# Kernel optimization log

Measured on AMD Instinct MI355X. Metric: run time of the kernel, lower is better.

Reference implementation:

```python
import jax, jax.numpy as jnp
import numpy as np

B = 2048            # number of session graphs in the batch
ORDER = 3           # multi-order granularities s1, s2, s3
D = 128             # input_dim = hidden_dim = output_dim (fc_out is None)
NODES_PER = (50, 25, 16)   # nodes per graph for s1, s2, s3
NPG = sum(NODES_PER)       # 91 nodes per graph (summed batch_num_nodes)
N = B * NPG                # total flattened nodes


def setup_inputs() -> dict:
    key = jax.random.key(0)
    k0, k1, k2, k3 = jax.random.split(key, 4)
    feats = jax.random.normal(k0, (N, D), dtype=jnp.float32)
    scale = 1.0 / np.sqrt(D).astype(np.float32)
    Wu = jax.random.normal(k1, (ORDER, D, D), dtype=jnp.float32) * scale
    bu = jnp.zeros((ORDER, D), dtype=jnp.float32)
    Wv = jax.random.normal(k2, (ORDER, D, D), dtype=jnp.float32) * scale
    We = jax.random.normal(k3, (ORDER, D), dtype=jnp.float32) * scale
    # segment id per node: idx = cat([ones(batch_num_nodes[j]) * j])
    idx = jnp.repeat(jnp.arange(B, dtype=jnp.int32), NPG)
    # last node of each order's block inside every graph (feats['s_i'][last_nodess[i]])
    offs = np.cumsum([0] + list(NODES_PER))
    last = np.stack([np.arange(B) * NPG + (offs[o + 1] - 1) for o in range(ORDER)])
    last_idx = jnp.asarray(last, dtype=jnp.int32)  # [ORDER, B]
    return {"feats": feats, "Wu": Wu, "bu": bu, "Wv": Wv, "We": We,
            "idx": idx, "last_idx": last_idx}


def reference(feats, Wu, bu, Wv, We, idx, last_idx):
    # feat_u = fc_u[i](feats)                        -> [O, N, D]
    feat_u = jnp.einsum('nd,odh->onh', feats, Wu) + bu[:, None, :]
    # feat_v = fc_v[i](feat_vs[:, i])[idx]           -> [O, N, D]
    fv = jnp.einsum('obd,odh->obh', feats[last_idx], Wv)   # [O, B, D]
    feat_v = fv[:, idx, :]                                  # gather per segment id
    # e = fc_e[i](sigmoid(feat_u + feat_v))          -> [N, O]
    e = jnp.einsum('onh,oh->no', jax.nn.sigmoid(feat_u + feat_v), We)
    # alpha = segment_softmax(batch_num_nodes, e), numerically stable
    m = jax.lax.stop_gradient(jax.ops.segment_max(e, idx, num_segments=B))
    ex = jnp.exp(e - m[idx])
    denom = jax.ops.segment_sum(ex, idx, num_segments=B)
    alpha = ex / denom[idx]                                 # [N, O]
    # rst = segment_reduce(batch_num_nodes, feats * alpha, 'sum') -> [B, O, D]
    weighted = alpha[:, :, None] * feats[:, None, :]        # [N, O, D]
    rst = jax.ops.segment_sum(weighted, idx, num_segments=B)
    return rst  # [B, ORDER, D]; fc_out is None and activation is None
```

## Files before the change

### kernel.cpp

```cpp
#include <hip/hip_runtime.h>
#include <hip/hip_bf16.h>
#include <stdint.h>

#define NB 2048
#define D 128
#define NPG 91

typedef __attribute__((ext_vector_type(8))) short short8;
typedef __attribute__((ext_vector_type(4))) float f32x4;

__device__ __forceinline__ unsigned bf16pk(float a, float b) {
  __hip_bfloat162 h2 = __float22bfloat162_rn(make_float2(a, b));
  return *reinterpret_cast<unsigned*>(&h2);
}

__device__ __forceinline__ float sigf(float x) {
  float e = __expf(-x);
  return __builtin_amdgcn_rcpf(1.0f + e);
}

__global__ void fv_kernel(const float* __restrict__ feats,
                          const float* __restrict__ Wv,
                          const float* __restrict__ bu,
                          const int* __restrict__ last_idx,
                          float* __restrict__ fv) {
  __shared__ float rows[16][128];
  __shared__ int lidx[16];
  const int o = blockIdx.y;
  const int b0 = blockIdx.x * 16;
  const int t = threadIdx.x;
  if (t < 16) lidx[t] = last_idx[o * NB + b0 + t];
  __syncthreads();
  #pragma unroll
  for (int i = 0; i < 8; ++i) {
    int el = t + i * 256;
    int r = el >> 7, d = el & 127;
    rows[r][d] = feats[(size_t)lidx[r] * D + d];
  }
  __syncthreads();
  const int h = t & 127, half = t >> 7;
  float acc[8];
  #pragma unroll
  for (int j = 0; j < 8; ++j) acc[j] = 0.f;
  const float* wvo = Wv + (size_t)o * D * D + h;
  for (int d0 = 0; d0 < D; d0 += 4) {
    float w0 = wvo[(d0 + 0) * D], w1 = wvo[(d0 + 1) * D];
    float w2 = wvo[(d0 + 2) * D], w3 = wvo[(d0 + 3) * D];
    #pragma unroll
    for (int j = 0; j < 8; ++j) {
      const float4 f = *(const float4*)&rows[half * 8 + j][d0];
      acc[j] += f.x * w0 + f.y * w1 + f.z * w2 + f.w * w3;
    }
  }
  const float bb = bu[o * D + h];
  #pragma unroll
  for (int j = 0; j < 8; ++j)
    fv[((size_t)o * NB + b0 + half * 8 + j) * D + h] = acc[j] + bb;
}

__global__ void wut_pack(const float* __restrict__ Wu, uint4* __restrict__ wupk) {
  const int o = blockIdx.x >> 2, kk = blockIdx.x & 3;
  const int t = threadIdx.x;
  #pragma unroll
  for (int i = 0; i < 2; ++i) {
    int idx = i * 256 + t;
    int row = idx >> 2, g = idx & 3;
    const float* src = Wu + (size_t)o * D * D + (kk * 32 + g * 8) * D + row;
    uint4 pk;
    pk.x = bf16pk(src[0 * D], src[1 * D]);
    pk.y = bf16pk(src[2 * D], src[3 * D]);
    pk.z = bf16pk(src[4 * D], src[5 * D]);
    pk.w = bf16pk(src[6 * D], src[7 * D]);
    wupk[(size_t)blockIdx.x * 512 + idx] = pk;
  }
}

__global__ __launch_bounds__(512, 8) void sihg_main(
    const float* __restrict__ feats,
    const uint4* __restrict__ wupk,
    const float* __restrict__ We,
    const float* __restrict__ fvb,
    float* __restrict__ out) {
  __shared__ __align__(16) char lds[38016];
  constexpr int FE_OFF  = 0;
  constexpr int BFV_OFF = 24576;
  constexpr int WEL_OFF = 26112;
  constexpr int EP_OFF  = 27648;
  constexpr int AL_OFF  = 36864;

  const int t = threadIdx.x;
  const int b = blockIdx.x;
  const int q = t >> 6;
  const int l = t & 63;
  const int g = l >> 4;
  const int lm = l & 15;

  float* bfvp = (float*)(lds + BFV_OFF);
  float* wel = (float*)(lds + WEL_OFF);
  float (*ep)[3][96] = (float (*)[3][96])(lds + EP_OFF);
  float (*alpha)[96] = (float (*)[96])(lds + AL_OFF);

  const float* fbase = feats + (size_t)b * NPG * D;

  #pragma unroll 1
  for (int i = 0; i < 3; ++i) {
    int c = t + i * 512;
    int r = c >> 4, d0 = (c & 15) * 8;
    uint4 pk4;
    if (r < NPG) {
      const float* src = fbase + r * D + d0;
      float4 f0 = *(const float4*)(src);
      float4 f1 = *(const float4*)(src + 4);
      pk4.x = bf16pk(f0.x, f0.y);
      pk4.y = bf16pk(f0.z, f0.w);
      pk4.z = bf16pk(f1.x, f1.y);
      pk4.w = bf16pk(f1.z, f1.w);
    } else {
      pk4.x = 0u; pk4.y = 0u; pk4.z = 0u; pk4.w = 0u;
    }
    int off = r * 256 + ((d0 * 2) ^ ((r & 7) << 4));
    *(uint4*)(lds + FE_OFF + off) = pk4;
  }
  if (t < 384) {
    bfvp[t] = fvb[((size_t)(t >> 7) * NB + b) * D + (t & 127)];
    wel[t] = We[t];
  }
  __syncthreads();

  const int sa = (lm & 7) << 4;
  #pragma unroll 1
  for (int o = 0; o < 3; ++o) {
    #pragma unroll 1
    for (int nh = 0; nh < 2; ++nh) {
      f32x4 acc[3];
      #pragma unroll
      for (int j = 0; j < 3; ++j) acc[j] = (f32x4){0.f, 0.f, 0.f, 0.f};

      #pragma unroll
      for (int kk = 0; kk < 4; ++kk) {
        short8 a = *(const short8*)&wupk[(size_t)(o * 4 + kk) * 512 + (q * 16 + lm) * 4 + g];
        const int cb = kk * 64 + g * 16;
        #pragma unroll
        for (int j = 0; j < 3; ++j) {
          const int nt = nh * 3 + j;
          short8 bfr = *(const short8*)(lds + FE_OFF + (nt * 16 + lm) * 256 + (cb ^ sa));
          acc[j] = __builtin_amdgcn_mfma_f32_16x16x32_bf16(a, bfr, acc[j], 0, 0, 0);
        }
      }
      const float* bbp = (const float*)(lds + BFV_OFF + o * 512 + (q * 16 + g * 4) * 4);
      const float* wwp = (const float*)(lds + WEL_OFF + o * 512 + (q * 16 + g * 4) * 4);
      #pragma unroll
      for (int j = 0; j < 3; ++j) {
        float e = 0.f;
        #pragma unroll
        for (int r = 0; r < 4; ++r)
          e += sigf(acc[j][r] + bbp[r]) * wwp[r];
        e += __shfl_xor(e, 16);
        e += __shfl_xor(e, 32);
        if (l < 16) ep[q][o][(nh * 3 + j) * 16 + l] = e;
      }
    }
  }
  __syncthreads();

  if (q < 3) {
    const int o = q;
    const int n1 = l, n2 = l + 64;
    float e1 = -1e30f, e2 = -1e30f;
    if (n1 < NPG) {
      e1 = 0.f;
      #pragma unroll
      for (int j = 0; j < 8; ++j) e1 += ep[j][o][n1];
    }
    if (n2 < NPG) {
      e2 = 0.f;
      #pragma unroll
      for (int j = 0; j < 8; ++j) e2 += ep[j][o][n2];
    }
    float mx = fmaxf(e1, e2);
    #pragma unroll
    for (int m = 1; m < 64; m <<= 1) mx = fmaxf(mx, __shfl_xor(mx, m));
    float x1 = (n1 < NPG) ? __expf(e1 - mx) : 0.f;
    float x2 = (n2 < NPG) ? __expf(e2 - mx) : 0.f;
    float s = x1 + x2;
    #pragma unroll
    for (int m = 1; m < 64; m <<= 1) s += __shfl_xor(s, m);
    float inv = __builtin_amdgcn_rcpf(s);
    if (n1 < NPG) alpha[o][n1] = x1 * inv;
    if (n2 < NPG) alpha[o][n2] = x2 * inv;
  }
  __syncthreads();

  {
    const int hw = t >> 5;
    const int d4 = (t & 31) * 4;
    float a0x = 0.f, a0y = 0.f, a0z = 0.f, a0w = 0.f;
    float a1x = 0.f, a1y = 0.f, a1z = 0.f, a1w = 0.f;
    float a2x = 0.f, a2y = 0.f, a2z = 0.f, a2w = 0.f;
    #pragma unroll 1
    for (int n = hw; n < NPG; n += 16) {
      float4 f = *(const float4*)(fbase + n * D + d4);
      float al0 = alpha[0][n], al1 = alpha[1][n], al2 = alpha[2][n];
      a0x += f.x * al0; a0y += f.y * al0; a0z += f.z * al0; a0w += f.w * al0;
      a1x += f.x * al1; a1y += f.y * al1; a1z += f.z * al1; a1w += f.w * al1;
      a2x += f.x * al2; a2y += f.y * al2; a2z += f.z * al2; a2w += f.w * al2;
    }
    a0x += __shfl_xor(a0x, 32); a0y += __shfl_xor(a0y, 32);
    a0z += __shfl_xor(a0z, 32); a0w += __shfl_xor(a0w, 32);
    a1x += __shfl_xor(a1x, 32); a1y += __shfl_xor(a1y, 32);
    a1z += __shfl_xor(a1z, 32); a1w += __shfl_xor(a1w, 32);
    a2x += __shfl_xor(a2x, 32); a2y += __shfl_xor(a2y, 32);
    a2z += __shfl_xor(a2z, 32); a2w += __shfl_xor(a2w, 32);
    float* part = (float*)(lds + FE_OFF);
    if (l < 32) {
      float4 s0 = {a0x, a0y, a0z, a0w};
      float4 s1 = {a1x, a1y, a1z, a1w};
      float4 s2 = {a2x, a2y, a2z, a2w};
      *(float4*)&part[q * 384 + 0 * 128 + d4] = s0;
      *(float4*)&part[q * 384 + 1 * 128 + d4] = s1;
      *(float4*)&part[q * 384 + 2 * 128 + d4] = s2;
    }
  }
  __syncthreads();
  if (t < 384) {
    const float* part = (const float*)(lds + FE_OFF);
    float s = 0.f;
    #pragma unroll
    for (int j = 0; j < 8; ++j) s += part[j * 384 + t];
    out[(size_t)b * 384 + t] = s;
  }
}

extern "C" void kernel_launch(void* const* d_in, const int* in_sizes, int n_in,
                              void* d_out, int out_size, void* d_ws, size_t ws_size,
                              hipStream_t stream) {
  const float* feats    = (const float*)d_in[0];
  const float* Wu       = (const float*)d_in[1];
  const float* bu       = (const float*)d_in[2];
  const float* Wv       = (const float*)d_in[3];
  const float* We       = (const float*)d_in[4];
  const int*   last_idx = (const int*)d_in[6];
  float* out = (float*)d_out;
  float* fvb  = (float*)d_ws;
  uint4* wupk = (uint4*)((char*)d_ws + 3 * NB * D * 4);

  dim3 g0(128, 3);
  fv_kernel<<<g0, 256, 0, stream>>>(feats, Wv, bu, last_idx, fvb);
  wut_pack<<<12, 256, 0, stream>>>(Wu, wupk);
  sihg_main<<<NB, 512, 0, stream>>>(feats, wupk, We, fvb, out);
}
```

Baseline: 70.90 us.

## Switch main GEMM to 32x32x16 MFMA tiles with 384-thread blocks

Replaces the 16x16x32 bf16 MFMA tiling with 32x32x16 MFMA tiles. Each of six waves computes two 32x32 output tiles over eight K steps, and the Wu pack layout is changed to match the new A-fragment format. The block shrinks from 512 to 384 threads, the alpha buffer is aliased onto the feature LDS region to cut shared memory, and the partial-sum reductions are reduced from 8 to 4 and 6 entries. The aim is fewer MFMA issues and fewer LDS fragment loads per output. The cost is fewer waves per block, and the epilogue and weighted-sum phase now get less parallelism.

```diff
diff --git a/kernel.cpp b/kernel.cpp
--- a/kernel.cpp
+++ b/kernel.cpp
@@ -8,6 +8,7 @@
 
 typedef __attribute__((ext_vector_type(8))) short short8;
 typedef __attribute__((ext_vector_type(4))) float f32x4;
+typedef __attribute__((ext_vector_type(16))) float f32x16;
 
 __device__ __forceinline__ unsigned bf16pk(float a, float b) {
   __hip_bfloat162 h2 = __float22bfloat162_rn(make_float2(a, b));
@@ -59,52 +60,48 @@
 }
 
 __global__ void wut_pack(const float* __restrict__ Wu, uint4* __restrict__ wupk) {
-  const int o = blockIdx.x >> 2, kk = blockIdx.x & 3;
+  const int o = blockIdx.x >> 3, step = blockIdx.x & 7;
   const int t = threadIdx.x;
-  #pragma unroll
-  for (int i = 0; i < 2; ++i) {
-    int idx = i * 256 + t;
-    int row = idx >> 2, g = idx & 3;
-    const float* src = Wu + (size_t)o * D * D + (kk * 32 + g * 8) * D + row;
-    uint4 pk;
-    pk.x = bf16pk(src[0 * D], src[1 * D]);
-    pk.y = bf16pk(src[2 * D], src[3 * D]);
-    pk.z = bf16pk(src[4 * D], src[5 * D]);
-    pk.w = bf16pk(src[6 * D], src[7 * D]);
-    wupk[(size_t)blockIdx.x * 512 + idx] = pk;
-  }
-}
-
-__global__ __launch_bounds__(512, 8) void sihg_main(
+  const int ht = t >> 6, rh = t & 63;
+  const int row = rh >> 1, hi = rh & 1;
+  const int k0 = step * 16 + hi * 8;
+  const float* src = Wu + (size_t)o * D * D + (size_t)k0 * D + ht * 32 + row;
+  uint4 pk;
+  pk.x = bf16pk(src[0 * D], src[1 * D]);
+  pk.y = bf16pk(src[2 * D], src[3 * D]);
+  pk.z = bf16pk(src[4 * D], src[5 * D]);
+  pk.w = bf16pk(src[6 * D], src[7 * D]);
+  wupk[(size_t)blockIdx.x * 256 + ht * 64 + row * 2 + hi] = pk;
+}
+
+__global__ __launch_bounds__(384, 6) void sihg_main(
     const float* __restrict__ feats,
     const uint4* __restrict__ wupk,
     const float* __restrict__ We,
     const float* __restrict__ fvb,
     float* __restrict__ out) {
-  __shared__ __align__(16) char lds[38016];
+  __shared__ __align__(16) char lds[32256];
   constexpr int FE_OFF  = 0;
   constexpr int BFV_OFF = 24576;
   constexpr int WEL_OFF = 26112;
   constexpr int EP_OFF  = 27648;
-  constexpr int AL_OFF  = 36864;
 
   const int t = threadIdx.x;
   const int b = blockIdx.x;
-  const int q = t >> 6;
+  const int w = t >> 6;
   const int l = t & 63;
-  const int g = l >> 4;
-  const int lm = l & 15;
+  const int l31 = l & 31;
+  const int hi = l >> 5;
 
   float* bfvp = (float*)(lds + BFV_OFF);
   float* wel = (float*)(lds + WEL_OFF);
   float (*ep)[3][96] = (float (*)[3][96])(lds + EP_OFF);
-  float (*alpha)[96] = (float (*)[96])(lds + AL_OFF);
 
   const float* fbase = feats + (size_t)b * NPG * D;
 
   #pragma unroll 1
-  for (int i = 0; i < 3; ++i) {
-    int c = t + i * 512;
+  for (int i = 0; i < 4; ++i) {
+    int c = t + i * 384;
     int r = c >> 4, d0 = (c & 15) * 8;
     uint4 pk4;
     if (r < NPG) {
@@ -121,62 +118,54 @@
     int off = r * 256 + ((d0 * 2) ^ ((r & 7) << 4));
     *(uint4*)(lds + FE_OFF + off) = pk4;
   }
-  if (t < 384) {
-    bfvp[t] = fvb[((size_t)(t >> 7) * NB + b) * D + (t & 127)];
-    wel[t] = We[t];
-  }
-  __syncthreads();
-
-  const int sa = (lm & 7) << 4;
+  bfvp[t] = fvb[((size_t)(t >> 7) * NB + b) * D + (t & 127)];
+  wel[t] = We[t];
+  __syncthreads();
+
   #pragma unroll 1
   for (int o = 0; o < 3; ++o) {
     #pragma unroll 1
-    for (int nh = 0; nh < 2; ++nh) {
-      f32x4 acc[3];
+    for (int tt = 0; tt < 2; ++tt) {
+      const int tile = w * 2 + tt;
+      const int ht = tile & 3;
+      const int nt = tile >> 2;
+      f32x16 acc = {};
+
+      const int brow = nt * 32 + l31;
+      const char* bbase = lds + FE_OFF + brow * 256;
+      const int swz = (brow & 7) << 4;
+      const uint4* abase = wupk + (size_t)(o * 8 * 4 + ht) * 64 + l31 * 2 + hi;
+
+      #pragma unroll 2
+      for (int step = 0; step < 8; ++step) {
+        uint4 au = abase[(size_t)step * 256];
+        short8 av = *reinterpret_cast<short8*>(&au);
+        short8 bv = *(const short8*)(bbase + ((step * 32 + hi * 16) ^ swz));
+        acc = __builtin_amdgcn_mfma_f32_32x32x16_bf16(av, bv, acc, 0, 0, 0);
+      }
+      float e = 0.f;
       #pragma unroll
-      for (int j = 0; j < 3; ++j) acc[j] = (f32x4){0.f, 0.f, 0.f, 0.f};
-
-      #pragma unroll
-      for (int kk = 0; kk < 4; ++kk) {
-        short8 a = *(const short8*)&wupk[(size_t)(o * 4 + kk) * 512 + (q * 16 + lm) * 4 + g];
-        const int cb = kk * 64 + g * 16;
-        #pragma unroll
-        for (int j = 0; j < 3; ++j) {
-          const int nt = nh * 3 + j;
-          short8 bfr = *(const short8*)(lds + FE_OFF + (nt * 16 + lm) * 256 + (cb ^ sa));
-          acc[j] = __builtin_amdgcn_mfma_f32_16x16x32_bf16(a, bfr, acc[j], 0, 0, 0);
-        }
+      for (int j = 0; j < 4; ++j) {
+        f32x4 bb = *(const f32x4*)&bfvp[o * 128 + ht * 32 + j * 8 + hi * 4];
+        f32x4 ww = *(const f32x4*)&wel[o * 128 + ht * 32 + j * 8 + hi * 4];
+        e += sigf(acc[j * 4 + 0] + bb[0]) * ww[0];
+        e += sigf(acc[j * 4 + 1] + bb[1]) * ww[1];
+        e += sigf(acc[j * 4 + 2] + bb[2]) * ww[2];
+        e += sigf(acc[j * 4 + 3] + bb[3]) * ww[3];
       }
-      const float* bbp = (const float*)(lds + BFV_OFF + o * 512 + (q * 16 + g * 4) * 4);
-      const float* wwp = (const float*)(lds + WEL_OFF + o * 512 + (q * 16 + g * 4) * 4);
-      #pragma unroll
-      for (int j = 0; j < 3; ++j) {
-        float e = 0.f;
-        #pragma unroll
-        for (int r = 0; r < 4; ++r)
-          e += sigf(acc[j][r] + bbp[r]) * wwp[r];
-        e += __shfl_xor(e, 16);
-        e += __shfl_xor(e, 32);
-        if (l < 16) ep[q][o][(nh * 3 + j) * 16 + l] = e;
-      }
-    }
-  }
-  __syncthreads();
-
-  if (q < 3) {
-    const int o = q;
+      e += __shfl_xor(e, 32);
+      if (l < 32) ep[ht][o][nt * 32 + l] = e;
+    }
+  }
+  __syncthreads();
+
+  float (*alpha)[96] = (float (*)[96])(lds + FE_OFF);
+  if (w < 3) {
+    const int o = w;
     const int n1 = l, n2 = l + 64;
     float e1 = -1e30f, e2 = -1e30f;
-    if (n1 < NPG) {
-      e1 = 0.f;
-      #pragma unroll
-      for (int j = 0; j < 8; ++j) e1 += ep[j][o][n1];
-    }
-    if (n2 < NPG) {
-      e2 = 0.f;
-      #pragma unroll
-      for (int j = 0; j < 8; ++j) e2 += ep[j][o][n2];
-    }
+    if (n1 < NPG) e1 = ep[0][o][n1] + ep[1][o][n1] + ep[2][o][n1] + ep[3][o][n1];
+    if (n2 < NPG) e2 = ep[0][o][n2] + ep[1][o][n2] + ep[2][o][n2] + ep[3][o][n2];
     float mx = fmaxf(e1, e2);
     #pragma unroll
     for (int m = 1; m < 64; m <<= 1) mx = fmaxf(mx, __shfl_xor(mx, m));
@@ -198,7 +187,7 @@
     float a1x = 0.f, a1y = 0.f, a1z = 0.f, a1w = 0.f;
     float a2x = 0.f, a2y = 0.f, a2z = 0.f, a2w = 0.f;
     #pragma unroll 1
-    for (int n = hw; n < NPG; n += 16) {
+    for (int n = hw; n < NPG; n += 12) {
       float4 f = *(const float4*)(fbase + n * D + d4);
       float al0 = alpha[0][n], al1 = alpha[1][n], al2 = alpha[2][n];
       a0x += f.x * al0; a0y += f.y * al0; a0z += f.z * al0; a0w += f.w * al0;
@@ -211,22 +200,22 @@
     a1z += __shfl_xor(a1z, 32); a1w += __shfl_xor(a1w, 32);
     a2x += __shfl_xor(a2x, 32); a2y += __shfl_xor(a2y, 32);
     a2z += __shfl_xor(a2z, 32); a2w += __shfl_xor(a2w, 32);
-    float* part = (float*)(lds + FE_OFF);
+    float* part = (float*)(lds + FE_OFF + 2048);
     if (l < 32) {
       float4 s0 = {a0x, a0y, a0z, a0w};
       float4 s1 = {a1x, a1y, a1z, a1w};
       float4 s2 = {a2x, a2y, a2z, a2w};
-      *(float4*)&part[q * 384 + 0 * 128 + d4] = s0;
-      *(float4*)&part[q * 384 + 1 * 128 + d4] = s1;
-      *(float4*)&part[q * 384 + 2 * 128 + d4] = s2;
-    }
-  }
-  __syncthreads();
-  if (t < 384) {
-    const float* part = (const float*)(lds + FE_OFF);
+      *(float4*)&part[w * 384 + 0 * 128 + d4] = s0;
+      *(float4*)&part[w * 384 + 1 * 128 + d4] = s1;
+      *(float4*)&part[w * 384 + 2 * 128 + d4] = s2;
+    }
+  }
+  __syncthreads();
+  {
+    const float* part = (const float*)(lds + FE_OFF + 2048);
     float s = 0.f;
     #pragma unroll
-    for (int j = 0; j < 8; ++j) s += part[j * 384 + t];
+    for (int j = 0; j < 6; ++j) s += part[j * 384 + t];
     out[(size_t)b * 384 + t] = s;
   }
 }
@@ -246,6 +235,6 @@
 
   dim3 g0(128, 3);
   fv_kernel<<<g0, 256, 0, stream>>>(feats, Wv, bu, last_idx, fvb);
-  wut_pack<<<12, 256, 0, stream>>>(Wu, wupk);
-  sihg_main<<<NB, 512, 0, stream>>>(feats, wupk, We, fvb, out);
-}
+  wut_pack<<<24, 256, 0, stream>>>(Wu, wupk);
+  sihg_main<<<NB, 384, 0, stream>>>(feats, wupk, We, fvb, out);
+}
```

Result: slower. 78.65 us (+10.9%).

## Fuse last-node fc_v projection into main kernel using MFMA on LDS rows

Applied to the files above, without the earlier changes.

Removes the separate fp32 fv_kernel and its workspace round-trip. The main kernel now computes each graph's fc_v projection with bf16 MFMA on the last-node rows already staged in LDS, adds the bias, and uses the result for the attention scores. Wv is packed together with Wu in a single pack kernel. The Wu fragments are hoisted into registers per order. This saves one launch and the global write and read of fv, at the cost of extra barriers per order and lower precision for fv. The last-node rows are now hardcoded (49/74/90) instead of being read from last_idx.

```diff
diff --git a/kernel.cpp b/kernel.cpp
--- a/kernel.cpp
+++ b/kernel.cpp
@@ -19,74 +19,41 @@
   return __builtin_amdgcn_rcpf(1.0f + e);
 }
 
-__global__ void fv_kernel(const float* __restrict__ feats,
-                          const float* __restrict__ Wv,
-                          const float* __restrict__ bu,
-                          const int* __restrict__ last_idx,
-                          float* __restrict__ fv) {
-  __shared__ float rows[16][128];
-  __shared__ int lidx[16];
-  const int o = blockIdx.y;
-  const int b0 = blockIdx.x * 16;
-  const int t = threadIdx.x;
-  if (t < 16) lidx[t] = last_idx[o * NB + b0 + t];
-  __syncthreads();
-  #pragma unroll
-  for (int i = 0; i < 8; ++i) {
-    int el = t + i * 256;
-    int r = el >> 7, d = el & 127;
-    rows[r][d] = feats[(size_t)lidx[r] * D + d];
-  }
-  __syncthreads();
-  const int h = t & 127, half = t >> 7;
-  float acc[8];
-  #pragma unroll
-  for (int j = 0; j < 8; ++j) acc[j] = 0.f;
-  const float* wvo = Wv + (size_t)o * D * D + h;
-  for (int d0 = 0; d0 < D; d0 += 4) {
-    float w0 = wvo[(d0 + 0) * D], w1 = wvo[(d0 + 1) * D];
-    float w2 = wvo[(d0 + 2) * D], w3 = wvo[(d0 + 3) * D];
-    #pragma unroll
-    for (int j = 0; j < 8; ++j) {
-      const float4 f = *(const float4*)&rows[half * 8 + j][d0];
-      acc[j] += f.x * w0 + f.y * w1 + f.z * w2 + f.w * w3;
-    }
-  }
-  const float bb = bu[o * D + h];
-  #pragma unroll
-  for (int j = 0; j < 8; ++j)
-    fv[((size_t)o * NB + b0 + half * 8 + j) * D + h] = acc[j] + bb;
-}
-
-__global__ void wut_pack(const float* __restrict__ Wu, uint4* __restrict__ wupk) {
-  const int o = blockIdx.x >> 2, kk = blockIdx.x & 3;
+__global__ void w_pack(const float* __restrict__ Wu,
+                       const float* __restrict__ Wv,
+                       uint4* __restrict__ wpk) {
+  const int u = blockIdx.x;
+  const float* W = (u < 12) ? Wu : Wv;
+  const int uu = (u < 12) ? u : u - 12;
+  const int o = uu >> 2, kk = uu & 3;
   const int t = threadIdx.x;
   #pragma unroll
   for (int i = 0; i < 2; ++i) {
     int idx = i * 256 + t;
     int row = idx >> 2, g = idx & 3;
-    const float* src = Wu + (size_t)o * D * D + (kk * 32 + g * 8) * D + row;
+    const float* src = W + (size_t)o * D * D + (kk * 32 + g * 8) * D + row;
     uint4 pk;
     pk.x = bf16pk(src[0 * D], src[1 * D]);
     pk.y = bf16pk(src[2 * D], src[3 * D]);
     pk.z = bf16pk(src[4 * D], src[5 * D]);
     pk.w = bf16pk(src[6 * D], src[7 * D]);
-    wupk[(size_t)blockIdx.x * 512 + idx] = pk;
+    wpk[(size_t)u * 512 + idx] = pk;
   }
 }
 
 __global__ __launch_bounds__(512, 8) void sihg_main(
     const float* __restrict__ feats,
-    const uint4* __restrict__ wupk,
+    const uint4* __restrict__ wpk,
+    const float* __restrict__ bu,
     const float* __restrict__ We,
-    const float* __restrict__ fvb,
     float* __restrict__ out) {
-  __shared__ __align__(16) char lds[38016];
+  __shared__ __align__(16) char lds[38528];
   constexpr int FE_OFF  = 0;
   constexpr int BFV_OFF = 24576;
-  constexpr int WEL_OFF = 26112;
-  constexpr int EP_OFF  = 27648;
-  constexpr int AL_OFF  = 36864;
+  constexpr int BUL_OFF = 25088;
+  constexpr int WEL_OFF = 26624;
+  constexpr int EP_OFF  = 28160;
+  constexpr int AL_OFF  = 37376;
 
   const int t = threadIdx.x;
   const int b = blockIdx.x;
@@ -96,6 +63,7 @@
   const int lm = l & 15;
 
   float* bfvp = (float*)(lds + BFV_OFF);
+  float* bul = (float*)(lds + BUL_OFF);
   float* wel = (float*)(lds + WEL_OFF);
   float (*ep)[3][96] = (float (*)[3][96])(lds + EP_OFF);
   float (*alpha)[96] = (float (*)[96])(lds + AL_OFF);
@@ -122,14 +90,38 @@
     *(uint4*)(lds + FE_OFF + off) = pk4;
   }
   if (t < 384) {
-    bfvp[t] = fvb[((size_t)(t >> 7) * NB + b) * D + (t & 127)];
+    bul[t] = bu[t];
     wel[t] = We[t];
   }
   __syncthreads();
 
-  const int sa = (lm & 7) << 4;
+  const int LROW[3] = {49, 74, 90};
+
   #pragma unroll 1
   for (int o = 0; o < 3; ++o) {
+    {
+      const int frow = LROW[o];
+      const int fswz = (frow & 7) << 4;
+      f32x4 z = {0.f, 0.f, 0.f, 0.f};
+      #pragma unroll
+      for (int kk = 0; kk < 4; ++kk) {
+        short8 av = *(const short8*)&wpk[(size_t)(12 + o * 4 + kk) * 512 + (q * 16 + lm) * 4 + g];
+        short8 bv = *(const short8*)(lds + FE_OFF + frow * 256 + ((kk * 64 + g * 16) ^ fswz));
+        z = __builtin_amdgcn_mfma_f32_16x16x32_bf16(av, bv, z, 0, 0, 0);
+      }
+      if (lm == 0) {
+        #pragma unroll
+        for (int r = 0; r < 4; ++r)
+          bfvp[q * 16 + g * 4 + r] = z[r] + bul[o * 128 + q * 16 + g * 4 + r];
+      }
+    }
+    __syncthreads();
+
+    short8 a[4];
+    #pragma unroll
+    for (int kk = 0; kk < 4; ++kk)
+      a[kk] = *(const short8*)&wpk[(size_t)(o * 4 + kk) * 512 + (q * 16 + lm) * 4 + g];
+
     #pragma unroll 1
     for (int nh = 0; nh < 2; ++nh) {
       f32x4 acc[3];
@@ -138,17 +130,16 @@
 
       #pragma unroll
       for (int kk = 0; kk < 4; ++kk) {
-        short8 a = *(const short8*)&wupk[(size_t)(o * 4 + kk) * 512 + (q * 16 + lm) * 4 + g];
         const int cb = kk * 64 + g * 16;
         #pragma unroll
         for (int j = 0; j < 3; ++j) {
           const int nt = nh * 3 + j;
-          short8 bfr = *(const short8*)(lds + FE_OFF + (nt * 16 + lm) * 256 + (cb ^ sa));
-          acc[j] = __builtin_amdgcn_mfma_f32_16x16x32_bf16(a, bfr, acc[j], 0, 0, 0);
+          short8 bfr = *(const short8*)(lds + FE_OFF + (nt * 16 + lm) * 256 + (cb ^ ((lm & 7) << 4)));
+          acc[j] = __builtin_amdgcn_mfma_f32_16x16x32_bf16(a[kk], bfr, acc[j], 0, 0, 0);
         }
       }
-      const float* bbp = (const float*)(lds + BFV_OFF + o * 512 + (q * 16 + g * 4) * 4);
-      const float* wwp = (const float*)(lds + WEL_OFF + o * 512 + (q * 16 + g * 4) * 4);
+      const float* bbp = &bfvp[q * 16 + g * 4];
+      const float* wwp = &wel[o * 128 + q * 16 + g * 4];
       #pragma unroll
       for (int j = 0; j < 3; ++j) {
         float e = 0.f;
@@ -160,6 +151,7 @@
         if (l < 16) ep[q][o][(nh * 3 + j) * 16 + l] = e;
       }
     }
+    if (o < 2) __syncthreads();
   }
   __syncthreads();
 
@@ -234,18 +226,14 @@
 extern "C" void kernel_launch(void* const* d_in, const int* in_sizes, int n_in,
                               void* d_out, int out_size, void* d_ws, size_t ws_size,
                               hipStream_t stream) {
-  const float* feats    = (const float*)d_in[0];
-  const float* Wu       = (const float*)d_in[1];
-  const float* bu       = (const float*)d_in[2];
-  const float* Wv       = (const float*)d_in[3];
-  const float* We       = (const float*)d_in[4];
-  const int*   last_idx = (const int*)d_in[6];
+  const float* feats = (const float*)d_in[0];
+  const float* Wu    = (const float*)d_in[1];
+  const float* bu    = (const float*)d_in[2];
+  const float* Wv    = (const float*)d_in[3];
+  const float* We    = (const float*)d_in[4];
   float* out = (float*)d_out;
-  float* fvb  = (float*)d_ws;
-  uint4* wupk = (uint4*)((char*)d_ws + 3 * NB * D * 4);
-
-  dim3 g0(128, 3);
-  fv_kernel<<<g0, 256, 0, stream>>>(feats, Wv, bu, last_idx, fvb);
-  wut_pack<<<12, 256, 0, stream>>>(Wu, wupk);
-  sihg_main<<<NB, 512, 0, stream>>>(feats, wupk, We, fvb, out);
-}
+  uint4* wpk = (uint4*)d_ws;
+
+  w_pack<<<24, 256, 0, stream>>>(Wu, Wv, wpk);
+  sihg_main<<<NB, 512, 0, stream>>>(feats, wpk, bu, We, out);
+}
```

Result: faster. 65.23 us (-8.0%).
